# Performance work log

Hardware: AMD Instinct MI355X
Metric: run time of the kernel (lower is better)

## Reference

```python
import jax, jax.numpy as jnp
from jax import lax
import numpy as np

B = 128            # graphs
N = 2048           # nodes per graph (contiguous per graph)
DEG = 8            # avg degree
E = B * N * DEG    # 2,097,152 edges
F_IN = 64
K1 = int(np.ceil(0.8 * N))    # 1639, TopKPooling ratio=0.8
K2 = int(np.ceil(0.8 * K1))   # 1312


def setup_inputs() -> dict:
    key = jax.random.key(0)
    ks = jax.random.split(key, 20)
    # within-graph random edges: global index = graph_offset + local index
    epg = N * DEG  # edges per graph
    offs = (jnp.arange(B, dtype=jnp.int64) * N)[:, None]
    src = (jax.random.randint(ks[0], (B, epg), 0, N) + offs).reshape(-1)
    dst = (jax.random.randint(ks[1], (B, epg), 0, N) + offs).reshape(-1)
    edge_index = jnp.stack([src, dst]).astype(jnp.int64)
    batch = jnp.repeat(jnp.arange(B, dtype=jnp.int64), N)
    r = lambda k, s: jax.random.normal(k, s, dtype=jnp.float32)
    return {
        "x": r(ks[2], (B * N, F_IN)),
        "edge_index": edge_index,
        "edge_attr": jax.random.uniform(ks[3], (E,), dtype=jnp.float32),
        "batch": batch,
        "W1_rel": r(ks[4], (F_IN, 32)) / np.sqrt(F_IN),
        "b1": r(ks[5], (32,)) * 0.01,
        "W1_root": r(ks[6], (F_IN, 32)) / np.sqrt(F_IN),
        "p1_w": r(ks[7], (32,)),
        "W2_rel": r(ks[8], (32, 32)) / np.sqrt(32),
        "b2": r(ks[9], (32,)) * 0.01,
        "W2_root": r(ks[10], (32, 32)) / np.sqrt(32),
        "p2_w": r(ks[11], (32,)),
        "lin1_W": r(ks[12], (64, 32)) / 8.0,
        "lin1_b": r(ks[13], (32,)) * 0.01,
        "lin2_W": r(ks[14], (32, 16)) / np.sqrt(32),
        "lin2_b": r(ks[15], (16,)) * 0.01,
        "lin3_W": r(ks[16], (16, 2)) / 4.0,
        "lin3_b": r(ks[17], (2,)) * 0.01,
    }


def _graph_conv(x, src, dst, ew, W_rel, b, W_root, num_nodes):
    # PyG GraphConv: out_i = W_rel @ sum_j w_ji x_j + W_root @ x_i + b
    msg = x[src] * ew[:, None]                                   # [E, F]
    agg = jax.ops.segment_sum(msg, dst, num_segments=num_nodes)  # [N, F]
    return agg @ W_rel + b + x @ W_root


def _topk_pool(x, pw, nodes_per_graph, k):
    # PyG TopKPooling: score = tanh((x . w)/||w||); keep top-k per graph;
    # x_out = x[perm] * score[perm]
    score = jnp.tanh((x @ pw) / jnp.linalg.norm(pw))             # [B*n]
    _, idx = lax.top_k(score.reshape(B, nodes_per_graph), k)     # [B, k] local
    perm = (idx + (jnp.arange(B) * nodes_per_graph)[:, None]).reshape(-1)
    xp = x[perm] * score[perm][:, None]                          # [B*k, F]
    return xp, perm


def reference(x, edge_index, edge_attr, batch, W1_rel, b1, W1_root, p1_w,
              W2_rel, b2, W2_root, p2_w, lin1_W, lin1_b, lin2_W, lin2_b,
              lin3_W, lin3_b):
    src, dst = edge_index[0], edge_index[1]
    n0 = B * N
    # conv1 + pool1
    h = jax.nn.relu(_graph_conv(x, src, dst, edge_attr, W1_rel, b1, W1_root, n0))
    h, perm1 = _topk_pool(h, p1_w, N, K1)                        # [B*K1, 32]
    # filter_adj: keep edges with both endpoints selected, remap indices;
    # invalid edges get weight 0 (no contribution to segment_sum)
    mapping = jnp.full((n0,), -1, dtype=jnp.int32).at[perm1].set(
        jnp.arange(B * K1, dtype=jnp.int32))
    ns, nd = mapping[src], mapping[dst]
    valid = (ns >= 0) & (nd >= 0)
    ew2 = jnp.where(valid, edge_attr, 0.0)
    src2 = jnp.where(valid, ns, 0)
    dst2 = jnp.where(valid, nd, 0)
    hb = h.reshape(B, K1, 32)
    x1 = jnp.concatenate([hb.max(axis=1), hb.mean(axis=1)], axis=1)  # [B, 64]
    # conv2 + pool2
    h = jax.nn.relu(_graph_conv(h, src2, dst2, ew2, W2_rel, b2, W2_root, B * K1))
    h, _ = _topk_pool(h, p2_w, K1, K2)                           # [B*K2, 32]
    hb = h.reshape(B, K2, 32)
    x2 = jnp.concatenate([hb.max(axis=1), hb.mean(axis=1)], axis=1)  # [B, 64]
    # readout MLP (dropout is identity in eval mode)
    z = x1 + x2
    z = jax.nn.relu(z @ lin1_W + lin1_b)
    z = jax.nn.relu(z @ lin2_W + lin2_b)
    return jax.nn.log_softmax(z @ lin3_W + lin3_b, axis=-1)      # [B, 2]
```

## Files before the change

### kernel.cpp

```cpp
#include <hip/hip_runtime.h>
#include <hip/hip_fp16.h>
#include <math.h>

#define NNODES (128*2048)
#define NEDGES (NNODES*8)
#define NPG 2048
#define EPG (NPG*8)
#define HPG (EPG/2)
#define NGRAPH 128
#define KSEL1 1639
#define KSEL2 1312

__device__ __forceinline__ unsigned packh2(float a, float b) {
    __half2 h = __floats2half2_rn(a, b);
    return *reinterpret_cast<unsigned*>(&h);
}
__device__ __forceinline__ float2 unph2(unsigned u) {
    __half2 h = *reinterpret_cast<__half2*>(&u);
    return __half22float2(h);
}

__global__ __launch_bounds__(1024) void k_csr(
    const int* __restrict__ src, const int* __restrict__ dst,
    const float* __restrict__ ew, int2* __restrict__ meta,
    int2* __restrict__ edge_sorted)
{
    __shared__ int cnt[NPG];
    __shared__ int curs[NPG];
    __shared__ int wsum[1024];
    int t = threadIdx.x;
    int bid = blockIdx.x;
    int g = bid >> 1, part = bid & 1;
    const int ebase = g * EPG + part * HPG;
    int ds[8], ss[8]; float wws[8];
    #pragma unroll
    for (int j=0;j<8;++j) {
        int idx = ebase + t + 1024*j;
        ds[j] = dst[idx] & (NPG-1);
        ss[j] = src[idx];
        wws[j] = ew[idx];
    }
    for (int i = t; i < NPG; i += 1024) cnt[i] = 0;
    __syncthreads();
    #pragma unroll
    for (int j=0;j<8;++j) atomicAdd(&cnt[ds[j]], 1);
    __syncthreads();
    int base = t * 2;
    int l0 = cnt[base], l1 = cnt[base+1];
    int s0 = l0 + l1;
    wsum[t] = s0;
    __syncthreads();
    for (int off=1; off<1024; off<<=1) {
        int add = (t>=off)?wsum[t-off]:0;
        __syncthreads();
        wsum[t]+=add;
        __syncthreads();
    }
    int run = wsum[t]-s0;
    curs[base] = run; curs[base+1] = run + l0;
    __syncthreads();
    for (int i = t; i < NPG; i += 1024)
        meta[(size_t)part*NNODES + g*NPG + i] = make_int2(ebase + curs[i], cnt[i]);
    __syncthreads();
    #pragma unroll
    for (int j=0;j<8;++j) {
        int pos = atomicAdd(&curs[ds[j]], 1);
        edge_sorted[ebase + pos] = make_int2(ss[j], __float_as_int(wws[j]));
    }
}

#define XP 36
__global__ __launch_bounds__(256, 4) void k_gemm64(
    const float* __restrict__ x, const float* __restrict__ Wrel,
    const float* __restrict__ Wroot, const float* __restrict__ b,
    unsigned char* __restrict__ yb, unsigned char* __restrict__ seedb)
{
    __shared__ float xs[128*XP];
    __shared__ float wcat[64*64];
    __shared__ float bb[32];
    int t = threadIdx.x;
    for (int i = t; i < 64*64; i += 256) {
        int k = i >> 6, j = i & 63;
        wcat[i] = (j < 32) ? Wrel[k*32 + j] : Wroot[k*32 + (j-32)];
    }
    if (t < 32) bb[t] = b[t];
    size_t nb = (size_t)blockIdx.x * 128;
    int q = t >> 5, ng = t & 31;
    float acc[4][8];
    #pragma unroll
    for (int i=0;i<4;++i)
        #pragma unroll
        for (int j=0;j<8;++j) acc[i][j]=0.f;
    for (int half = 0; half < 2; ++half) {
        __syncthreads();
        const float* xg = x + nb*64 + half*32;
        for (int i = t; i < 128*8; i += 256) {
            int r = i >> 3, c = i & 7;
            *(float4*)(&xs[r*XP + c*4]) = *(const float4*)(xg + r*64 + c*4);
        }
        __syncthreads();
        int kb = half*32;
        #pragma unroll 2
        for (int k = 0; k < 32; k += 4) {
            float4 w0[4], w1[4];
            #pragma unroll
            for (int kk=0;kk<4;++kk) {
                w0[kk] = *(const float4*)(&wcat[(kb+k+kk)*64 + q*8]);
                w1[kk] = *(const float4*)(&wcat[(kb+k+kk)*64 + q*8 + 4]);
            }
            #pragma unroll
            for (int i=0;i<4;++i) {
                float4 xv = *(const float4*)(&xs[(ng + i*32)*XP + k]);
                float xvv[4] = {xv.x, xv.y, xv.z, xv.w};
                #pragma unroll
                for (int kk=0;kk<4;++kk) {
                    acc[i][0]=fmaf(xvv[kk], w0[kk].x, acc[i][0]);
                    acc[i][1]=fmaf(xvv[kk], w0[kk].y, acc[i][1]);
                    acc[i][2]=fmaf(xvv[kk], w0[kk].z, acc[i][2]);
                    acc[i][3]=fmaf(xvv[kk], w0[kk].w, acc[i][3]);
                    acc[i][4]=fmaf(xvv[kk], w1[kk].x, acc[i][4]);
                    acc[i][5]=fmaf(xvv[kk], w1[kk].y, acc[i][5]);
                    acc[i][6]=fmaf(xvv[kk], w1[kk].z, acc[i][6]);
                    acc[i][7]=fmaf(xvv[kk], w1[kk].w, acc[i][7]);
                }
            }
        }
    }
    if (q < 4) {
        #pragma unroll
        for (int i=0;i<4;++i) {
            uint4 pk;
            pk.x = packh2(acc[i][0], acc[i][1]);
            pk.y = packh2(acc[i][2], acc[i][3]);
            pk.z = packh2(acc[i][4], acc[i][5]);
            pk.w = packh2(acc[i][6], acc[i][7]);
            *(uint4*)(yb + (nb + ng + i*32)*64 + q*16) = pk;
        }
    } else {
        int qq = q - 4;
        float b0=bb[qq*8+0],b1=bb[qq*8+1],b2=bb[qq*8+2],b3=bb[qq*8+3];
        float b4=bb[qq*8+4],b5=bb[qq*8+5],b6=bb[qq*8+6],b7=bb[qq*8+7];
        #pragma unroll
        for (int i=0;i<4;++i) {
            uint4 pk;
            pk.x = packh2(acc[i][0]+b0, acc[i][1]+b1);
            pk.y = packh2(acc[i][2]+b2, acc[i][3]+b3);
            pk.z = packh2(acc[i][4]+b4, acc[i][5]+b5);
            pk.w = packh2(acc[i][6]+b6, acc[i][7]+b7);
            *(uint4*)(seedb + (nb + ng + i*32)*64 + qq*16) = pk;
        }
    }
}

__global__ __launch_bounds__(256, 4) void k_gemm32(
    const unsigned char* __restrict__ hb, const float* __restrict__ ts,
    const float* __restrict__ Wrel, const float* __restrict__ Wroot,
    const float* __restrict__ b, unsigned char* __restrict__ yb,
    unsigned char* __restrict__ seedb)
{
    __shared__ float xs[128*XP];
    __shared__ float wcat[32*64];
    __shared__ float bb[32];
    int t = threadIdx.x;
    for (int i = t; i < 32*64; i += 256) {
        int k = i >> 6, j = i & 63;
        wcat[i] = (j < 32) ? Wrel[k*32 + j] : Wroot[k*32 + (j-32)];
    }
    if (t < 32) bb[t] = b[t];
    size_t nb = (size_t)blockIdx.x * 128;
    const unsigned char* hg = hb + nb * 64;
    for (int i = t; i < 128*4; i += 256) {
        int r = i >> 2, c = i & 3;
        uint4 u = *(const uint4*)(hg + r*64 + c*16);
        float2 p0=unph2(u.x), p1=unph2(u.y), p2=unph2(u.z), p3=unph2(u.w);
        float* dst = &xs[r*XP + c*8];
        *(float4*)(dst)   = make_float4(p0.x,p0.y,p1.x,p1.y);
        *(float4*)(dst+4) = make_float4(p2.x,p2.y,p3.x,p3.y);
    }
    __syncthreads();
    int q = t >> 5, ng = t & 31;
    float tsv[4];
    #pragma unroll
    for (int i=0;i<4;++i) tsv[i] = ts[nb + ng + i*32];
    float acc[4][8];
    #pragma unroll
    for (int i=0;i<4;++i)
        #pragma unroll
        for (int j=0;j<8;++j) acc[i][j]=0.f;
    #pragma unroll 2
    for (int k = 0; k < 32; k += 4) {
        float4 w0[4], w1[4];
        #pragma unroll
        for (int kk=0;kk<4;++kk) {
            w0[kk] = *(const float4*)(&wcat[(k+kk)*64 + q*8]);
            w1[kk] = *(const float4*)(&wcat[(k+kk)*64 + q*8 + 4]);
        }
        #pragma unroll
        for (int i=0;i<4;++i) {
            float4 xv = *(const float4*)(&xs[(ng + i*32)*XP + k]);
            float xvv[4] = {xv.x, xv.y, xv.z, xv.w};
            #pragma unroll
            for (int kk=0;kk<4;++kk) {
                acc[i][0]=fmaf(xvv[kk], w0[kk].x, acc[i][0]);
                acc[i][1]=fmaf(xvv[kk], w0[kk].y, acc[i][1]);
                acc[i][2]=fmaf(xvv[kk], w0[kk].z, acc[i][2]);
                acc[i][3]=fmaf(xvv[kk], w0[kk].w, acc[i][3]);
                acc[i][4]=fmaf(xvv[kk], w1[kk].x, acc[i][4]);
                acc[i][5]=fmaf(xvv[kk], w1[kk].y, acc[i][5]);
                acc[i][6]=fmaf(xvv[kk], w1[kk].z, acc[i][6]);
                acc[i][7]=fmaf(xvv[kk], w1[kk].w, acc[i][7]);
            }
        }
    }
    if (q < 4) {
        #pragma unroll
        for (int i=0;i<4;++i) {
            float sc = tsv[i];
            uint4 pk;
            pk.x = packh2(acc[i][0]*sc, acc[i][1]*sc);
            pk.y = packh2(acc[i][2]*sc, acc[i][3]*sc);
            pk.z = packh2(acc[i][4]*sc, acc[i][5]*sc);
            pk.w = packh2(acc[i][6]*sc, acc[i][7]*sc);
            *(uint4*)(yb + (nb + ng + i*32)*64 + q*16) = pk;
        }
    } else {
        int qq = q - 4;
        float b0=bb[qq*8+0],b1=bb[qq*8+1],b2=bb[qq*8+2],b3=bb[qq*8+3];
        float b4=bb[qq*8+4],b5=bb[qq*8+5],b6=bb[qq*8+6],b7=bb[qq*8+7];
        #pragma unroll
        for (int i=0;i<4;++i) {
            float sc = tsv[i];
            uint4 pk;
            pk.x = packh2(acc[i][0]*sc+b0, acc[i][1]*sc+b1);
            pk.y = packh2(acc[i][2]*sc+b2, acc[i][3]*sc+b3);
            pk.z = packh2(acc[i][4]*sc+b4, acc[i][5]*sc+b5);
            pk.w = packh2(acc[i][6]*sc+b6, acc[i][7]*sc+b7);
            *(uint4*)(seedb + (nb + ng + i*32)*64 + qq*16) = pk;
        }
    }
}

__global__ __launch_bounds__(256) void k_gather(
    const int2* __restrict__ meta, const int2* __restrict__ edge_sorted,
    const unsigned char* __restrict__ yb, const float* __restrict__ pw,
    const int* __restrict__ mask, const unsigned char* __restrict__ seedb,
    unsigned char* __restrict__ hout, float* __restrict__ s)
{
    unsigned orig = blockIdx.x;
    unsigned nwg8 = gridDim.x >> 3;
    unsigned bid = (orig & 7u) * nwg8 + (orig >> 3);
    size_t tid = (size_t)bid * 256 + threadIdx.x;
    int node = (int)(tid >> 2);
    int q = (int)(tid & 3);
    float4 wv0 = ((const float4*)pw)[2*q];
    float4 wv1 = ((const float4*)pw)[2*q+1];
    float nn = wv0.x*wv0.x + wv0.y*wv0.y + wv0.z*wv0.z + wv0.w*wv0.w
             + wv1.x*wv1.x + wv1.y*wv1.y + wv1.z*wv1.z + wv1.w*wv1.w;
    nn += __shfl_xor(nn, 1); nn += __shfl_xor(nn, 2);
    float nrm = sqrtf(nn);
    bool valid = mask ? (mask[node] != 0) : true;
    float4 a0 = make_float4(0.f,0.f,0.f,0.f), a1 = make_float4(0.f,0.f,0.f,0.f);
    float4 b0 = make_float4(0.f,0.f,0.f,0.f), b1 = make_float4(0.f,0.f,0.f,0.f);
    if (valid) {
        uint4 su = *(const uint4*)(seedb + (size_t)node * 64 + q * 16);
        float2 s0 = unph2(su.x), s1 = unph2(su.y), s2 = unph2(su.z), s3 = unph2(su.w);
        a0 = make_float4(s0.x, s0.y, s1.x, s1.y);
        a1 = make_float4(s2.x, s2.y, s3.x, s3.y);
        #pragma unroll
        for (int p = 0; p < 2; ++p) {
            int2 m = meta[(size_t)p*NNODES + node];
            int e = m.x, end = m.x + m.y;
            for (; e + 1 < end; e += 2) {
                int2 ed0 = edge_sorted[e];
                int2 ed1 = edge_sorted[e+1];
                uint4 u0 = *(const uint4*)(yb + (size_t)ed0.x * 64 + q * 16);
                uint4 u1 = *(const uint4*)(yb + (size_t)ed1.x * 64 + q * 16);
                float w0 = __int_as_float(ed0.y);
                float w1 = __int_as_float(ed1.y);
                float2 p0, p1;
                p0 = unph2(u0.x); p1 = unph2(u0.y);
                a0.x = fmaf(p0.x, w0, a0.x); a0.y = fmaf(p0.y, w0, a0.y);
                a0.z = fmaf(p1.x, w0, a0.z); a0.w = fmaf(p1.y, w0, a0.w);
                p0 = unph2(u0.z); p1 = unph2(u0.w);
                a1.x = fmaf(p0.x, w0, a1.x); a1.y = fmaf(p0.y, w0, a1.y);
                a1.z = fmaf(p1.x, w0, a1.z); a1.w = fmaf(p1.y, w0, a1.w);
                p0 = unph2(u1.x); p1 = unph2(u1.y);
                b0.x = fmaf(p0.x, w1, b0.x); b0.y = fmaf(p0.y, w1, b0.y);
                b0.z = fmaf(p1.x, w1, b0.z); b0.w = fmaf(p1.y, w1, b0.w);
                p0 = unph2(u1.z); p1 = unph2(u1.w);
                b1.x = fmaf(p0.x, w1, b1.x); b1.y = fmaf(p0.y, w1, b1.y);
                b1.z = fmaf(p1.x, w1, b1.z); b1.w = fmaf(p1.y, w1, b1.w);
            }
            if (e < end) {
                int2 ed0 = edge_sorted[e];
                uint4 u0 = *(const uint4*)(yb + (size_t)ed0.x * 64 + q * 16);
                float w0 = __int_as_float(ed0.y);
                float2 p0, p1;
                p0 = unph2(u0.x); p1 = unph2(u0.y);
                a0.x = fmaf(p0.x, w0, a0.x); a0.y = fmaf(p0.y, w0, a0.y);
                a0.z = fmaf(p1.x, w0, a0.z); a0.w = fmaf(p1.y, w0, a0.w);
                p0 = unph2(u0.z); p1 = unph2(u0.w);
                a1.x = fmaf(p0.x, w0, a1.x); a1.y = fmaf(p0.y, w0, a1.y);
                a1.z = fmaf(p1.x, w0, a1.z); a1.w = fmaf(p1.y, w0, a1.w);
            }
        }
    }
    float hv0x = fmaxf(a0.x + b0.x, 0.f), hv0y = fmaxf(a0.y + b0.y, 0.f);
    float hv0z = fmaxf(a0.z + b0.z, 0.f), hv0w = fmaxf(a0.w + b0.w, 0.f);
    float hv1x = fmaxf(a1.x + b1.x, 0.f), hv1y = fmaxf(a1.y + b1.y, 0.f);
    float hv1z = fmaxf(a1.z + b1.z, 0.f), hv1w = fmaxf(a1.w + b1.w, 0.f);
    uint4 hw;
    hw.x = packh2(hv0x, hv0y);
    hw.y = packh2(hv0z, hv0w);
    hw.z = packh2(hv1x, hv1y);
    hw.w = packh2(hv1z, hv1w);
    *(uint4*)(hout + (size_t)node * 64 + q * 16) = hw;
    float dot = hv0x*wv0.x + hv0y*wv0.y + hv0z*wv0.z + hv0w*wv0.w
              + hv1x*wv1.x + hv1y*wv1.y + hv1z*wv1.z + hv1w*wv1.w;
    dot += __shfl_xor(dot, 1); dot += __shfl_xor(dot, 2);
    if (q == 0) s[node] = valid ? (dot / nrm) : -INFINITY;
}

__global__ __launch_bounds__(1024) void k_pool(
    const float* __restrict__ s, const unsigned char* __restrict__ hb,
    float* __restrict__ ts_out, int* __restrict__ mask_out,
    float* __restrict__ xout, int ksel)
{
    __shared__ unsigned keys[NPG];
    __shared__ unsigned hist[256];
    __shared__ unsigned scanb[256];
    __shared__ unsigned tiescan[1024];
    __shared__ unsigned char flag[NPG];
    __shared__ unsigned sh_bin, sh_krem;
    __shared__ float red[16*64];
    int t = threadIdx.x;
    int g = blockIdx.x;
    const float* sg = s + (size_t)g * NPG;
    for (int i = t; i < NPG; i += 1024) {
        unsigned u = __float_as_uint(sg[i]);
        keys[i] = (u & 0x80000000u) ? ~u : (u | 0x80000000u);
    }
    __syncthreads();
    unsigned prefix = 0u;
    unsigned krem = (unsigned)ksel;
    for (int level = 0; level < 4; ++level) {
        int shift = 24 - 8*level;
        if (t < 256) hist[t] = 0u;
        __syncthreads();
        unsigned pmask = level ? (0xFFFFFFFFu << (shift + 8)) : 0u;
        for (int i = t; i < NPG; i += 1024) {
            unsigned key = keys[i];
            if ((key & pmask) == prefix)
                atomicAdd(&hist[(key >> shift) & 0xFFu], 1u);
        }
        __syncthreads();
        if (t < 256) scanb[t] = hist[255 - t];
        __syncthreads();
        for (int off = 1; off < 256; off <<= 1) {
            unsigned add = (t < 256 && t >= off) ? scanb[t - off] : 0u;
            __syncthreads();
            if (t < 256) scanb[t] += add;
            __syncthreads();
        }
        if (t < 256) {
            unsigned incl = scanb[t];
            unsigned excl = t ? scanb[t-1] : 0u;
            if (incl >= krem && excl < krem) {
                sh_bin = (unsigned)(255 - t);
                sh_krem = krem - excl;
            }
        }
        __syncthreads();
        prefix |= (sh_bin << shift);
        krem = sh_krem;
        __syncthreads();
    }
    unsigned T = prefix;
    unsigned ties = krem;
    int base = t * 2;
    unsigned k0 = keys[base], k1 = keys[base+1];
    unsigned ceq = (k0 == T ? 1u : 0u) + (k1 == T ? 1u : 0u);
    tiescan[t] = ceq;
    __syncthreads();
    for (int off = 1; off < 1024; off <<= 1) {
        unsigned add = (t >= off) ? tiescan[t - off] : 0u;
        __syncthreads();
        tiescan[t] += add;
        __syncthreads();
    }
    unsigned run = tiescan[t] - ceq;
    {
        unsigned char f0, f1;
        if (k0 > T) f0 = 1;
        else if (k0 == T) { f0 = (run < ties) ? 1 : 0; run++; }
        else f0 = 0;
        if (k1 > T) f1 = 1;
        else if (k1 == T) { f1 = (run < ties) ? 1 : 0; run++; }
        else f1 = 0;
        flag[base] = f0; flag[base+1] = f1;
    }
    __syncthreads();

    float mx[32], sm[32];
    #pragma unroll
    for (int j=0;j<32;++j){ mx[j]=-INFINITY; sm[j]=0.f; }
    const unsigned char* hg = hb + (size_t)g * NPG * 64;
    for (int i = t; i < NPG; i += 1024) {
        bool sel = flag[i] != 0;
        float tsv = sel ? tanhf(sg[i]) : 0.f;
        const uint4* hr = (const uint4*)(hg + (size_t)i*64);
        #pragma unroll
        for (int c4=0;c4<4;++c4) {
            uint4 u = hr[c4];
            float2 p0=unph2(u.x), p1=unph2(u.y), p2=unph2(u.z), p3=unph2(u.w);
            float vals[8] = {p0.x,p0.y,p1.x,p1.y,p2.x,p2.y,p3.x,p3.y};
            #pragma unroll
            for (int j=0;j<8;++j) {
                float v = vals[j]*tsv;
                if (sel) { mx[c4*8+j]=fmaxf(mx[c4*8+j],v); sm[c4*8+j]+=v; }
            }
        }
        if (ts_out) ts_out[(size_t)g*NPG + i] = tsv;
        if (mask_out) mask_out[(size_t)g*NPG + i] = sel ? 1 : 0;
    }
    #pragma unroll
    for (int j=0;j<32;++j) {
        for (int off=32; off; off>>=1) {
            mx[j] = fmaxf(mx[j], __shfl_xor(mx[j], off));
            sm[j] += __shfl_xor(sm[j], off);
        }
    }
    int wave = t >> 6, lane = t & 63;
    if (lane == 0) {
        #pragma unroll
        for (int j=0;j<32;++j) { red[wave*64 + j] = mx[j]; red[wave*64 + 32 + j] = sm[j]; }
    }
    __syncthreads();
    if (t < 32) {
        float m = red[t], ss = red[32 + t];
        #pragma unroll
        for (int w=1; w<16; ++w) { m = fmaxf(m, red[w*64 + t]); ss += red[w*64 + 32 + t]; }
        xout[(size_t)g*64 + t] = m;
        xout[(size_t)g*64 + 32 + t] = ss / (float)ksel;
    }
}

__global__ __launch_bounds__(128) void k_readout(
    const float* __restrict__ x1, const float* __restrict__ x2,
    const float* __restrict__ l1W, const float* __restrict__ l1b,
    const float* __restrict__ l2W, const float* __restrict__ l2b,
    const float* __restrict__ l3W, const float* __restrict__ l3b,
    float* __restrict__ out)
{
    int g = threadIdx.x;
    float z[64];
    #pragma unroll
    for (int i=0;i<64;++i) z[i] = x1[g*64+i] + x2[g*64+i];
    float a1[32];
    for (int j=0;j<32;++j) {
        float acc = l1b[j];
        #pragma unroll
        for (int i=0;i<64;++i) acc = fmaf(z[i], l1W[i*32+j], acc);
        a1[j] = fmaxf(acc, 0.f);
    }
    float a2[16];
    for (int j=0;j<16;++j) {
        float acc = l2b[j];
        #pragma unroll
        for (int i=0;i<32;++i) acc = fmaf(a1[i], l2W[i*16+j], acc);
        a2[j] = fmaxf(acc, 0.f);
    }
    float o0 = l3b[0], o1 = l3b[1];
    #pragma unroll
    for (int i=0;i<16;++i) { o0 = fmaf(a2[i], l3W[i*2+0], o0); o1 = fmaf(a2[i], l3W[i*2+1], o1); }
    float m = fmaxf(o0, o1);
    float lse = m + logf(expf(o0-m) + expf(o1-m));
    out[g*2+0] = o0 - lse;
    out[g*2+1] = o1 - lse;
}

extern "C" void kernel_launch(void* const* d_in, const int* in_sizes, int n_in,
                              void* d_out, int out_size, void* d_ws, size_t ws_size,
                              hipStream_t stream)
{
    const float* x      = (const float*)d_in[0];
    const int*   ei     = (const int*)d_in[1];
    const float* eattr  = (const float*)d_in[2];
    const float* W1rel  = (const float*)d_in[4];
    const float* b1     = (const float*)d_in[5];
    const float* W1root = (const float*)d_in[6];
    const float* p1w    = (const float*)d_in[7];
    const float* W2rel  = (const float*)d_in[8];
    const float* b2     = (const float*)d_in[9];
    const float* W2root = (const float*)d_in[10];
    const float* p2w    = (const float*)d_in[11];
    const float* l1W    = (const float*)d_in[12];
    const float* l1b    = (const float*)d_in[13];
    const float* l2W    = (const float*)d_in[14];
    const float* l2b    = (const float*)d_in[15];
    const float* l3W    = (const float*)d_in[16];
    const float* l3b    = (const float*)d_in[17];
    const int* srcp = ei;
    const int* dstp = ei + NEDGES;

    unsigned char* yb    = (unsigned char*)d_ws;
    unsigned char* seedb = yb + (size_t)NNODES*64;
    unsigned char* hb    = seedb + (size_t)NNODES*64;
    float* s1   = (float*)(hb + (size_t)NNODES*64);
    float* ts   = s1 + NNODES;
    int*   mask = (int*)(ts + NNODES);
    float* x1   = (float*)(mask + NNODES);
    float* x2   = x1 + NGRAPH*64;
    int2*  meta = (int2*)(x2 + NGRAPH*64);
    int2*  edge_sorted = (int2*)(meta + 2*NNODES);
    float* out  = (float*)d_out;

    dim3 b256(256);
    k_csr<<<NGRAPH*2, dim3(1024), 0, stream>>>(srcp, dstp, eattr, meta,
                                               edge_sorted);
    k_gemm64<<<NNODES/128, b256, 0, stream>>>(x, W1rel, W1root, b1, yb, seedb);
    k_gather<<<NNODES*4/256, b256, 0, stream>>>(meta, edge_sorted,
                                                yb, p1w, nullptr, seedb, hb, s1);
    k_pool<<<NGRAPH, dim3(1024), 0, stream>>>(s1, hb, ts, mask, x1, KSEL1);
    k_gemm32<<<NNODES/128, b256, 0, stream>>>(hb, ts, W2rel, W2root, b2, yb, seedb);
    k_gather<<<NNODES*4/256, b256, 0, stream>>>(meta, edge_sorted,
                                                yb, p2w, mask, seedb, hb, s1);
    k_pool<<<NGRAPH, dim3(1024), 0, stream>>>(s1, hb, nullptr, nullptr, x2, KSEL2);
    k_readout<<<1, 128, 0, stream>>>(x1, x2, l1W, l1b, l2W, l2b, l3W, l3b, out);
}
```

Measured before the change: 219.6 us.

## Stage per-graph projected features in LDS for edge gather

The gather kernel now runs two 1024-thread blocks per graph. Each block first copies the whole graph's 2048×64-byte feature table into shared memory with a rotated-chunk swizzle, then each thread processes four nodes, reading neighbour rows from LDS instead of issuing random global loads. Because edges stay inside a graph, the local index is recovered with a mask. The trade is 128 KB of LDS per block, which limits occupancy to about one block per CU, and each graph's table is loaded twice. There are also only 256 blocks, fewer than before, which may leave latency less well hidden.

```diff
diff --git a/kernel.cpp b/kernel.cpp
--- a/kernel.cpp
+++ b/kernel.cpp
@@ -240,85 +240,100 @@
     }
 }
 
-__global__ __launch_bounds__(256) void k_gather(
+__global__ __launch_bounds__(1024) void k_gather(
     const int2* __restrict__ meta, const int2* __restrict__ edge_sorted,
     const unsigned char* __restrict__ yb, const float* __restrict__ pw,
     const int* __restrict__ mask, const unsigned char* __restrict__ seedb,
     unsigned char* __restrict__ hout, float* __restrict__ s)
 {
-    unsigned orig = blockIdx.x;
-    unsigned nwg8 = gridDim.x >> 3;
-    unsigned bid = (orig & 7u) * nwg8 + (orig >> 3);
-    size_t tid = (size_t)bid * 256 + threadIdx.x;
-    int node = (int)(tid >> 2);
-    int q = (int)(tid & 3);
+    __shared__ unsigned char ylds[NPG*64];
+    int t = threadIdx.x;
+    int bid = blockIdx.x;
+    int g = bid >> 1, half = bid & 1;
+    {
+        const unsigned char* yg = yb + (size_t)g * (NPG*64);
+        #pragma unroll
+        for (int j = 0; j < 8; ++j) {
+            int i = t + 1024*j;
+            int n = i >> 2, c = i & 3;
+            *(uint4*)(&ylds[n*64 + (((c + n) & 3) << 4)]) =
+                *(const uint4*)(yg + (size_t)i * 16);
+        }
+    }
+    __syncthreads();
+    int q = t & 3;
     float4 wv0 = ((const float4*)pw)[2*q];
     float4 wv1 = ((const float4*)pw)[2*q+1];
     float nn = wv0.x*wv0.x + wv0.y*wv0.y + wv0.z*wv0.z + wv0.w*wv0.w
              + wv1.x*wv1.x + wv1.y*wv1.y + wv1.z*wv1.z + wv1.w*wv1.w;
     nn += __shfl_xor(nn, 1); nn += __shfl_xor(nn, 2);
     float nrm = sqrtf(nn);
-    bool valid = mask ? (mask[node] != 0) : true;
-    float4 a0 = make_float4(0.f,0.f,0.f,0.f), a1 = make_float4(0.f,0.f,0.f,0.f);
-    float4 b0 = make_float4(0.f,0.f,0.f,0.f), b1 = make_float4(0.f,0.f,0.f,0.f);
-    if (valid) {
-        uint4 su = *(const uint4*)(seedb + (size_t)node * 64 + q * 16);
-        float2 s0 = unph2(su.x), s1 = unph2(su.y), s2 = unph2(su.z), s3 = unph2(su.w);
-        a0 = make_float4(s0.x, s0.y, s1.x, s1.y);
-        a1 = make_float4(s2.x, s2.y, s3.x, s3.y);
-        #pragma unroll
-        for (int p = 0; p < 2; ++p) {
-            int2 m = meta[(size_t)p*NNODES + node];
-            int e = m.x, end = m.x + m.y;
-            for (; e + 1 < end; e += 2) {
-                int2 ed0 = edge_sorted[e];
-                int2 ed1 = edge_sorted[e+1];
-                uint4 u0 = *(const uint4*)(yb + (size_t)ed0.x * 64 + q * 16);
-                uint4 u1 = *(const uint4*)(yb + (size_t)ed1.x * 64 + q * 16);
-                float w0 = __int_as_float(ed0.y);
-                float w1 = __int_as_float(ed1.y);
-                float2 p0, p1;
-                p0 = unph2(u0.x); p1 = unph2(u0.y);
-                a0.x = fmaf(p0.x, w0, a0.x); a0.y = fmaf(p0.y, w0, a0.y);
-                a0.z = fmaf(p1.x, w0, a0.z); a0.w = fmaf(p1.y, w0, a0.w);
-                p0 = unph2(u0.z); p1 = unph2(u0.w);
-                a1.x = fmaf(p0.x, w0, a1.x); a1.y = fmaf(p0.y, w0, a1.y);
-                a1.z = fmaf(p1.x, w0, a1.z); a1.w = fmaf(p1.y, w0, a1.w);
-                p0 = unph2(u1.x); p1 = unph2(u1.y);
-                b0.x = fmaf(p0.x, w1, b0.x); b0.y = fmaf(p0.y, w1, b0.y);
-                b0.z = fmaf(p1.x, w1, b0.z); b0.w = fmaf(p1.y, w1, b0.w);
-                p0 = unph2(u1.z); p1 = unph2(u1.w);
-                b1.x = fmaf(p0.x, w1, b1.x); b1.y = fmaf(p0.y, w1, b1.y);
-                b1.z = fmaf(p1.x, w1, b1.z); b1.w = fmaf(p1.y, w1, b1.w);
+    for (int it = 0; it < 4; ++it) {
+        int node = g*NPG + half*1024 + it*256 + (t >> 2);
+        bool valid = mask ? (mask[node] != 0) : true;
+        float4 a0 = make_float4(0.f,0.f,0.f,0.f), a1 = make_float4(0.f,0.f,0.f,0.f);
+        float4 b0 = make_float4(0.f,0.f,0.f,0.f), b1 = make_float4(0.f,0.f,0.f,0.f);
+        if (valid) {
+            uint4 su = *(const uint4*)(seedb + (size_t)node * 64 + q * 16);
+            float2 s0 = unph2(su.x), s1 = unph2(su.y), s2 = unph2(su.z), s3 = unph2(su.w);
+            a0 = make_float4(s0.x, s0.y, s1.x, s1.y);
+            a1 = make_float4(s2.x, s2.y, s3.x, s3.y);
+            #pragma unroll
+            for (int p = 0; p < 2; ++p) {
+                int2 m = meta[(size_t)p*NNODES + node];
+                int e = m.x, end = m.x + m.y;
+                for (; e + 1 < end; e += 2) {
+                    int2 ed0 = edge_sorted[e];
+                    int2 ed1 = edge_sorted[e+1];
+                    int l0 = ed0.x & (NPG-1), l1 = ed1.x & (NPG-1);
+                    uint4 u0 = *(const uint4*)(&ylds[l0*64 + (((q + l0) & 3) << 4)]);
+                    uint4 u1 = *(const uint4*)(&ylds[l1*64 + (((q + l1) & 3) << 4)]);
+                    float w0 = __int_as_float(ed0.y);
+                    float w1 = __int_as_float(ed1.y);
+                    float2 p0, p1;
+                    p0 = unph2(u0.x); p1 = unph2(u0.y);
+                    a0.x = fmaf(p0.x, w0, a0.x); a0.y = fmaf(p0.y, w0, a0.y);
+                    a0.z = fmaf(p1.x, w0, a0.z); a0.w = fmaf(p1.y, w0, a0.w);
+                    p0 = unph2(u0.z); p1 = unph2(u0.w);
+                    a1.x = fmaf(p0.x, w0, a1.x); a1.y = fmaf(p0.y, w0, a1.y);
+                    a1.z = fmaf(p1.x, w0, a1.z); a1.w = fmaf(p1.y, w0, a1.w);
+                    p0 = unph2(u1.x); p1 = unph2(u1.y);
+                    b0.x = fmaf(p0.x, w1, b0.x); b0.y = fmaf(p0.y, w1, b0.y);
+                    b0.z = fmaf(p1.x, w1, b0.z); b0.w = fmaf(p1.y, w1, b0.w);
+                    p0 = unph2(u1.z); p1 = unph2(u1.w);
+                    b1.x = fmaf(p0.x, w1, b1.x); b1.y = fmaf(p0.y, w1, b1.y);
+                    b1.z = fmaf(p1.x, w1, b1.z); b1.w = fmaf(p1.y, w1, b1.w);
+                }
+                if (e < end) {
+                    int2 ed0 = edge_sorted[e];
+                    int l0 = ed0.x & (NPG-1);
+                    uint4 u0 = *(const uint4*)(&ylds[l0*64 + (((q + l0) & 3) << 4)]);
+                    float w0 = __int_as_float(ed0.y);
+                    float2 p0, p1;
+                    p0 = unph2(u0.x); p1 = unph2(u0.y);
+                    a0.x = fmaf(p0.x, w0, a0.x); a0.y = fmaf(p0.y, w0, a0.y);
+                    a0.z = fmaf(p1.x, w0, a0.z); a0.w = fmaf(p1.y, w0, a0.w);
+                    p0 = unph2(u0.z); p1 = unph2(u0.w);
+                    a1.x = fmaf(p0.x, w0, a1.x); a1.y = fmaf(p0.y, w0, a1.y);
+                    a1.z = fmaf(p1.x, w0, a1.z); a1.w = fmaf(p1.y, w0, a1.w);
+                }
             }
-            if (e < end) {
-                int2 ed0 = edge_sorted[e];
-                uint4 u0 = *(const uint4*)(yb + (size_t)ed0.x * 64 + q * 16);
-                float w0 = __int_as_float(ed0.y);
-                float2 p0, p1;
-                p0 = unph2(u0.x); p1 = unph2(u0.y);
-                a0.x = fmaf(p0.x, w0, a0.x); a0.y = fmaf(p0.y, w0, a0.y);
-                a0.z = fmaf(p1.x, w0, a0.z); a0.w = fmaf(p1.y, w0, a0.w);
-                p0 = unph2(u0.z); p1 = unph2(u0.w);
-                a1.x = fmaf(p0.x, w0, a1.x); a1.y = fmaf(p0.y, w0, a1.y);
-                a1.z = fmaf(p1.x, w0, a1.z); a1.w = fmaf(p1.y, w0, a1.w);
-            }
-        }
-    }
-    float hv0x = fmaxf(a0.x + b0.x, 0.f), hv0y = fmaxf(a0.y + b0.y, 0.f);
-    float hv0z = fmaxf(a0.z + b0.z, 0.f), hv0w = fmaxf(a0.w + b0.w, 0.f);
-    float hv1x = fmaxf(a1.x + b1.x, 0.f), hv1y = fmaxf(a1.y + b1.y, 0.f);
-    float hv1z = fmaxf(a1.z + b1.z, 0.f), hv1w = fmaxf(a1.w + b1.w, 0.f);
-    uint4 hw;
-    hw.x = packh2(hv0x, hv0y);
-    hw.y = packh2(hv0z, hv0w);
-    hw.z = packh2(hv1x, hv1y);
-    hw.w = packh2(hv1z, hv1w);
-    *(uint4*)(hout + (size_t)node * 64 + q * 16) = hw;
-    float dot = hv0x*wv0.x + hv0y*wv0.y + hv0z*wv0.z + hv0w*wv0.w
-              + hv1x*wv1.x + hv1y*wv1.y + hv1z*wv1.z + hv1w*wv1.w;
-    dot += __shfl_xor(dot, 1); dot += __shfl_xor(dot, 2);
-    if (q == 0) s[node] = valid ? (dot / nrm) : -INFINITY;
+        }
+        float hv0x = fmaxf(a0.x + b0.x, 0.f), hv0y = fmaxf(a0.y + b0.y, 0.f);
+        float hv0z = fmaxf(a0.z + b0.z, 0.f), hv0w = fmaxf(a0.w + b0.w, 0.f);
+        float hv1x = fmaxf(a1.x + b1.x, 0.f), hv1y = fmaxf(a1.y + b1.y, 0.f);
+        float hv1z = fmaxf(a1.z + b1.z, 0.f), hv1w = fmaxf(a1.w + b1.w, 0.f);
+        uint4 hw;
+        hw.x = packh2(hv0x, hv0y);
+        hw.y = packh2(hv0z, hv0w);
+        hw.z = packh2(hv1x, hv1y);
+        hw.w = packh2(hv1z, hv1w);
+        *(uint4*)(hout + (size_t)node * 64 + q * 16) = hw;
+        float dot = hv0x*wv0.x + hv0y*wv0.y + hv0z*wv0.z + hv0w*wv0.w
+                  + hv1x*wv1.x + hv1y*wv1.y + hv1z*wv1.z + hv1w*wv1.w;
+        dot += __shfl_xor(dot, 1); dot += __shfl_xor(dot, 2);
+        if (q == 0) s[node] = valid ? (dot / nrm) : -INFINITY;
+    }
 }
 
 __global__ __launch_bounds__(1024) void k_pool(
@@ -519,12 +534,12 @@
     k_csr<<<NGRAPH*2, dim3(1024), 0, stream>>>(srcp, dstp, eattr, meta,
                                                edge_sorted);
     k_gemm64<<<NNODES/128, b256, 0, stream>>>(x, W1rel, W1root, b1, yb, seedb);
-    k_gather<<<NNODES*4/256, b256, 0, stream>>>(meta, edge_sorted,
-                                                yb, p1w, nullptr, seedb, hb, s1);
+    k_gather<<<NGRAPH*2, dim3(1024), 0, stream>>>(meta, edge_sorted,
+                                                  yb, p1w, nullptr, seedb, hb, s1);
     k_pool<<<NGRAPH, dim3(1024), 0, stream>>>(s1, hb, ts, mask, x1, KSEL1);
     k_gemm32<<<NNODES/128, b256, 0, stream>>>(hb, ts, W2rel, W2root, b2, yb, seedb);
-    k_gather<<<NNODES*4/256, b256, 0, stream>>>(meta, edge_sorted,
-                                                yb, p2w, mask, seedb, hb, s1);
+    k_gather<<<NGRAPH*2, dim3(1024), 0, stream>>>(meta, edge_sorted,
+                                                  yb, p2w, mask, seedb, hb, s1);
     k_pool<<<NGRAPH, dim3(1024), 0, stream>>>(s1, hb, nullptr, nullptr, x2, KSEL2);
     k_readout<<<1, 128, 0, stream>>>(x1, x2, l1W, l1b, l2W, l2b, l3W, l3b, out);
 }
```

Result: no change. 222.6 us (+1.4%).
